# Kernel tuning notes

Hardware: AMD Instinct MI355X
Metric: run time of the kernel (lower is better)

## Reference

```python
import jax, jax.numpy as jnp
import numpy as np

B, C, N, T = 16, 32, 128, 12
C_OUT = 64


def setup_inputs() -> dict:
    key = jax.random.key(0)
    k1, k2, k3 = jax.random.split(key, 3)
    x = jax.random.normal(k1, (B, C, N, T), dtype=jnp.float32)
    # dynamic adjacency: per batch, per input channel, per timestep graph [B,C,N,N,T]
    A = jax.random.normal(k2, (B, C, N, N, T), dtype=jnp.float32) * 0.1
    # 1x1 conv over concat of order-1 and order-2 propagations: c_in_total = 2*1*C
    W = jax.random.normal(k3, (C_OUT, 2 * C), dtype=jnp.float32) * (1.0 / np.sqrt(2 * C))
    b = jnp.zeros((C_OUT,), dtype=jnp.float32)
    return {"x": x, "A": A, "W": W, "b": b}


def reference(x, A, W, b):
    # dynamic_nconv: contract node dim j against per-(b,channel,time) adjacency
    x1 = jnp.einsum('bijl,bijkl->bikl', x, A)    # order-1 propagation [B,C,N,T]
    x2 = jnp.einsum('bijl,bijkl->bikl', x1, A)   # order-2 propagation [B,C,N,T]
    h = jnp.concatenate([x1, x2], axis=1)        # [B, 2C, N, T]
    # 1x1 Conv2d == channel-mixing matmul; dropout is identity at inference
    out = jnp.einsum('oc,bcnl->bonl', W, h) + b[None, :, None, None]
    return out
```

## Files before the change

### kernel.cpp

```cpp
#include <hip/hip_runtime.h>
#include <stdint.h>


#define NN 128
#define TT 12
#define KL 1536
#define KLV 384
#define CHUNK4 (NN * KLV)

__global__ __launch_bounds__(768) void gcn_prop_kernel(
    const float4* __restrict__ A4,
    const float4* __restrict__ x4,
    float4* __restrict__ h4)
{
    __shared__ float4 xs[KLV];
    __shared__ float4 x1s[KLV];
    __shared__ float4 psum[768];
    const int t = threadIdx.x;
    const int half = (t >= KLV);
    const int th = t - half * KLV;
    const int la4 = th % 3;
    const int j0 = half * 64;

    for (int rep = 0; rep < 2; ++rep) {
        const int cid = blockIdx.x + rep * 256;
        const int bb = cid >> 5;
        const int ii = cid & 31;
        const float4* Ab = A4 + (size_t)cid * CHUNK4 + th;

        if (t < KLV) xs[t] = x4[cid * KLV + t];
        __syncthreads();

        float4 acc = make_float4(0.f, 0.f, 0.f, 0.f);
        #pragma unroll 8
        for (int jj = 0; jj < 64; ++jj) {
            const int j = j0 + jj;
            float4 a  = Ab[j * KLV];
            float4 xv = xs[j * 3 + la4];
            acc.x = fmaf(xv.x, a.x, acc.x);
            acc.y = fmaf(xv.y, a.y, acc.y);
            acc.z = fmaf(xv.z, a.z, acc.z);
            acc.w = fmaf(xv.w, a.w, acc.w);
        }
        psum[t] = acc;
        __syncthreads();
        if (t < KLV) {
            float4 p0 = psum[t], p1 = psum[t + KLV];
            float4 tot = make_float4(p0.x + p1.x, p0.y + p1.y,
                                     p0.z + p1.z, p0.w + p1.w);
            x1s[t] = tot;
            h4[(size_t)(bb * 64 + ii) * KLV + t] = tot;
        }
        __syncthreads();

        float4 acc2 = make_float4(0.f, 0.f, 0.f, 0.f);
        #pragma unroll 8
        for (int jj = 0; jj < 64; ++jj) {
            const int j = j0 + 63 - jj;
            float4 a  = Ab[j * KLV];
            float4 xv = x1s[j * 3 + la4];
            acc2.x = fmaf(xv.x, a.x, acc2.x);
            acc2.y = fmaf(xv.y, a.y, acc2.y);
            acc2.z = fmaf(xv.z, a.z, acc2.z);
            acc2.w = fmaf(xv.w, a.w, acc2.w);
        }
        psum[t] = acc2;
        __syncthreads();
        if (t < KLV) {
            float4 p0 = psum[t], p1 = psum[t + KLV];
            float4 tot = make_float4(p0.x + p1.x, p0.y + p1.y,
                                     p0.z + p1.z, p0.w + p1.w);
            h4[(size_t)(bb * 64 + 32 + ii) * KLV + t] = tot;
        }
        __syncthreads();
    }
}

__global__ __launch_bounds__(384) void mix_kernel(
    const float4* __restrict__ h4,
    const float* __restrict__ W,
    const float* __restrict__ bias,
    float4* __restrict__ out4)
{
    __shared__ float wsm[8][64];
    __shared__ float bsm[8];
    const int t = threadIdx.x;
    const int b  = blockIdx.x >> 3;
    const int o0 = (blockIdx.x & 7) * 8;
    {
        const int o = t >> 6, c = t & 63;
        if (t < 384) wsm[o][c] = W[(o0 + o) * 64 + c];
    }
    if (t < 128) {
        const int o = 6 + (t >> 6), c = t & 63;
        wsm[o][c] = W[(o0 + o) * 64 + c];
    }
    if (t < 8) bsm[t] = bias[o0 + t];
    __syncthreads();

    float4 acc[8];
    #pragma unroll
    for (int o = 0; o < 8; ++o) {
        const float bv = bsm[o];
        acc[o] = make_float4(bv, bv, bv, bv);
    }
    const float4* hb = h4 + (size_t)b * 64 * KLV + t;
    for (int c = 0; c < 64; ++c) {
        float4 hv = hb[(size_t)c * KLV];
        #pragma unroll
        for (int o = 0; o < 8; ++o) {
            const float w = wsm[o][c];
            acc[o].x = fmaf(w, hv.x, acc[o].x);
            acc[o].y = fmaf(w, hv.y, acc[o].y);
            acc[o].z = fmaf(w, hv.z, acc[o].z);
            acc[o].w = fmaf(w, hv.w, acc[o].w);
        }
    }
    #pragma unroll
    for (int o = 0; o < 8; ++o)
        out4[(size_t)(b * 64 + o0 + o) * KLV + t] = acc[o];
}

extern "C" void kernel_launch(void* const* d_in, const int* in_sizes, int n_in,
                              void* d_out, int out_size, void* d_ws, size_t ws_size,
                              hipStream_t stream) {
    const float4* x4 = (const float4*)d_in[0];
    const float4* A4 = (const float4*)d_in[1];
    const float*  W  = (const float*)d_in[2];
    const float*  bs = (const float*)d_in[3];
    float4* h4   = (float4*)d_ws;
    float4* out4 = (float4*)d_out;

    gcn_prop_kernel<<<dim3(256), dim3(768), 0, stream>>>(A4, x4, h4);
    mix_kernel<<<dim3(128), dim3(384), 0, stream>>>(h4, W, bs, out4);
}
```

Before: 593.2 us.

## Interleave second chunk's first-order pass with first chunk's second-order pass

The propagation kernel now processes its two (batch, channel) chunks in a software-pipelined order. The first-order pass of chunk 1 is fused into the same loop as the second-order pass of chunk 0. Each iteration then has two independent streams of A loads in flight, which should raise memory-level parallelism and remove one barrier phase. The cost is more shared memory and more registers per thread, which could lower occupancy. A redundant bounds check in the mix kernel is also dropped.

Result: no change. 591.8 us (-0.2%).

```diff
diff --git a/kernel.cpp b/kernel.cpp
--- a/kernel.cpp
+++ b/kernel.cpp
@@ -13,66 +13,107 @@
     const float4* __restrict__ x4,
     float4* __restrict__ h4)
 {
-    __shared__ float4 xs[KLV];
-    __shared__ float4 x1s[KLV];
-    __shared__ float4 psum[768];
+    __shared__ float4 xs0[KLV];
+    __shared__ float4 xs1[KLV];
+    __shared__ float4 x1s0[KLV];
+    __shared__ float4 x1s1[KLV];
+    __shared__ float4 ps0[768];
+    __shared__ float4 ps1[768];
+
     const int t = threadIdx.x;
     const int half = (t >= KLV);
     const int th = t - half * KLV;
     const int la4 = th % 3;
     const int j0 = half * 64;
 
-    for (int rep = 0; rep < 2; ++rep) {
-        const int cid = blockIdx.x + rep * 256;
-        const int bb = cid >> 5;
-        const int ii = cid & 31;
-        const float4* Ab = A4 + (size_t)cid * CHUNK4 + th;
+    const int cid0 = blockIdx.x;
+    const int cid1 = blockIdx.x + 256;
+    const int bb0 = cid0 >> 5, ii0 = cid0 & 31;
+    const int bb1 = cid1 >> 5, ii1 = cid1 & 31;
+    const float4* Ab0 = A4 + (size_t)cid0 * CHUNK4 + th;
+    const float4* Ab1 = A4 + (size_t)cid1 * CHUNK4 + th;
 
-        if (t < KLV) xs[t] = x4[cid * KLV + t];
-        __syncthreads();
+    if (t < KLV) {
+        xs0[t] = x4[cid0 * KLV + t];
+        xs1[t] = x4[cid1 * KLV + t];
+    }
+    __syncthreads();
 
-        float4 acc = make_float4(0.f, 0.f, 0.f, 0.f);
-        #pragma unroll 8
-        for (int jj = 0; jj < 64; ++jj) {
-            const int j = j0 + jj;
-            float4 a  = Ab[j * KLV];
-            float4 xv = xs[j * 3 + la4];
-            acc.x = fmaf(xv.x, a.x, acc.x);
-            acc.y = fmaf(xv.y, a.y, acc.y);
-            acc.z = fmaf(xv.z, a.z, acc.z);
-            acc.w = fmaf(xv.w, a.w, acc.w);
-        }
-        psum[t] = acc;
-        __syncthreads();
-        if (t < KLV) {
-            float4 p0 = psum[t], p1 = psum[t + KLV];
-            float4 tot = make_float4(p0.x + p1.x, p0.y + p1.y,
-                                     p0.z + p1.z, p0.w + p1.w);
-            x1s[t] = tot;
-            h4[(size_t)(bb * 64 + ii) * KLV + t] = tot;
-        }
-        __syncthreads();
+    float4 acc = make_float4(0.f, 0.f, 0.f, 0.f);
+    #pragma unroll 8
+    for (int jj = 0; jj < 64; ++jj) {
+        const int j = j0 + jj;
+        float4 a  = Ab0[j * KLV];
+        float4 xv = xs0[j * 3 + la4];
+        acc.x = fmaf(xv.x, a.x, acc.x);
+        acc.y = fmaf(xv.y, a.y, acc.y);
+        acc.z = fmaf(xv.z, a.z, acc.z);
+        acc.w = fmaf(xv.w, a.w, acc.w);
+    }
+    ps0[t] = acc;
+    __syncthreads();
+    if (t < KLV) {
+        float4 p0 = ps0[t], p1 = ps0[t + KLV];
+        float4 tot = make_float4(p0.x + p1.x, p0.y + p1.y,
+                                 p0.z + p1.z, p0.w + p1.w);
+        x1s0[t] = tot;
+        h4[(size_t)(bb0 * 64 + ii0) * KLV + t] = tot;
+    }
+    __syncthreads();
 
-        float4 acc2 = make_float4(0.f, 0.f, 0.f, 0.f);
-        #pragma unroll 8
-        for (int jj = 0; jj < 64; ++jj) {
-            const int j = j0 + 63 - jj;
-            float4 a  = Ab[j * KLV];
-            float4 xv = x1s[j * 3 + la4];
-            acc2.x = fmaf(xv.x, a.x, acc2.x);
-            acc2.y = fmaf(xv.y, a.y, acc2.y);
-            acc2.z = fmaf(xv.z, a.z, acc2.z);
-            acc2.w = fmaf(xv.w, a.w, acc2.w);
-        }
-        psum[t] = acc2;
-        __syncthreads();
-        if (t < KLV) {
-            float4 p0 = psum[t], p1 = psum[t + KLV];
-            float4 tot = make_float4(p0.x + p1.x, p0.y + p1.y,
-                                     p0.z + p1.z, p0.w + p1.w);
-            h4[(size_t)(bb * 64 + 32 + ii) * KLV + t] = tot;
-        }
-        __syncthreads();
+    float4 acc2 = make_float4(0.f, 0.f, 0.f, 0.f);
+    float4 acc1 = make_float4(0.f, 0.f, 0.f, 0.f);
+    #pragma unroll 4
+    for (int jj = 0; jj < 64; ++jj) {
+        const int jr = j0 + 63 - jj;
+        const int jf = j0 + jj;
+        float4 a2  = Ab0[jr * KLV];
+        float4 x2v = x1s0[jr * 3 + la4];
+        float4 a1  = Ab1[jf * KLV];
+        float4 x1v = xs1[jf * 3 + la4];
+        acc2.x = fmaf(x2v.x, a2.x, acc2.x);
+        acc2.y = fmaf(x2v.y, a2.y, acc2.y);
+        acc2.z = fmaf(x2v.z, a2.z, acc2.z);
+        acc2.w = fmaf(x2v.w, a2.w, acc2.w);
+        acc1.x = fmaf(x1v.x, a1.x, acc1.x);
+        acc1.y = fmaf(x1v.y, a1.y, acc1.y);
+        acc1.z = fmaf(x1v.z, a1.z, acc1.z);
+        acc1.w = fmaf(x1v.w, a1.w, acc1.w);
+    }
+    ps0[t] = acc2;
+    ps1[t] = acc1;
+    __syncthreads();
+    if (t < KLV) {
+        float4 q0 = ps0[t], q1 = ps0[t + KLV];
+        float4 tot2 = make_float4(q0.x + q1.x, q0.y + q1.y,
+                                  q0.z + q1.z, q0.w + q1.w);
+        h4[(size_t)(bb0 * 64 + 32 + ii0) * KLV + t] = tot2;
+        float4 r0 = ps1[t], r1 = ps1[t + KLV];
+        float4 tot1 = make_float4(r0.x + r1.x, r0.y + r1.y,
+                                  r0.z + r1.z, r0.w + r1.w);
+        x1s1[t] = tot1;
+        h4[(size_t)(bb1 * 64 + ii1) * KLV + t] = tot1;
+    }
+    __syncthreads();
+
+    float4 acc3 = make_float4(0.f, 0.f, 0.f, 0.f);
+    #pragma unroll 8
+    for (int jj = 0; jj < 64; ++jj) {
+        const int j = j0 + 63 - jj;
+        float4 a  = Ab1[j * KLV];
+        float4 xv = x1s1[j * 3 + la4];
+        acc3.x = fmaf(xv.x, a.x, acc3.x);
+        acc3.y = fmaf(xv.y, a.y, acc3.y);
+        acc3.z = fmaf(xv.z, a.z, acc3.z);
+        acc3.w = fmaf(xv.w, a.w, acc3.w);
+    }
+    ps0[t] = acc3;
+    __syncthreads();
+    if (t < KLV) {
+        float4 p0 = ps0[t], p1 = ps0[t + KLV];
+        float4 tot = make_float4(p0.x + p1.x, p0.y + p1.y,
+                                 p0.z + p1.z, p0.w + p1.w);
+        h4[(size_t)(bb1 * 64 + 32 + ii1) * KLV + t] = tot;
     }
 }
 
@@ -89,7 +130,7 @@
     const int o0 = (blockIdx.x & 7) * 8;
     {
         const int o = t >> 6, c = t & 63;
-        if (t < 384) wsm[o][c] = W[(o0 + o) * 64 + c];
+        wsm[o][c] = W[(o0 + o) * 64 + c];
     }
     if (t < 128) {
         const int o = 6 + (t >> 6), c = t & 63;
```
